# Optimization experiments

Measured on AMD Instinct MI355X. Metric: run time of the kernel, lower is better.

## Reference

```python
import jax, jax.numpy as jnp
import numpy as np

HEAD_SIZE = 64
N_EMBED = 1024
B, T = 8, 2048


def setup_inputs() -> dict:
    key = jax.random.key(0)
    ks = jax.random.split(key, 7)
    s = lambda fan_in: 1.0 / np.sqrt(fan_in)
    return {
        "x": jax.random.normal(ks[0], (B, T, N_EMBED), dtype=jnp.float32),
        # Linear weights stored as (in, out) so projection is x @ W + b
        "Wk": jax.random.uniform(ks[1], (N_EMBED, HEAD_SIZE), jnp.float32, -s(N_EMBED), s(N_EMBED)),
        "bk": jax.random.uniform(ks[2], (HEAD_SIZE,), jnp.float32, -s(N_EMBED), s(N_EMBED)),
        "Wq": jax.random.uniform(ks[3], (N_EMBED, HEAD_SIZE), jnp.float32, -s(N_EMBED), s(N_EMBED)),
        "bq": jax.random.uniform(ks[4], (HEAD_SIZE,), jnp.float32, -s(N_EMBED), s(N_EMBED)),
        "Wv": jax.random.uniform(ks[5], (N_EMBED, HEAD_SIZE), jnp.float32, -s(N_EMBED), s(N_EMBED)),
        "bv": jax.random.uniform(ks[6], (HEAD_SIZE,), jnp.float32, -s(N_EMBED), s(N_EMBED)),
    }


def reference(x, Wk, bk, Wq, bq, Wv, bv):
    Bb, Tt, C = x.shape
    k = x @ Wk + bk  # [B,T,H]
    q = x @ Wq + bq
    v = x @ Wv + bv
    # NOTE: original computes k @ q^T (keys as rows, queries as cols)
    wei = jnp.einsum("bth,bsh->bts", k, q) * (C ** -0.5)  # [B,T,T]
    causal = jnp.tril(jnp.ones((Tt, Tt), dtype=bool))
    wei = jnp.where(causal, wei, -jnp.inf)
    # softplus instead of softmax; softplus(-inf) = 0, stable via logaddexp
    wei = jnp.logaddexp(wei, 0.0)
    # dropout omitted (eval mode / deterministic reference)
    out = jnp.einsum("bts,bsh->bth", wei, v)  # [B,T,H]
    return out
```

## Files before the change

### kernel.cpp

```cpp
#include <hip/hip_runtime.h>
#include <hip/hip_bf16.h>
#include <stdint.h>

#define HEAD 64
#define CEMB 1024
#define BB 8
#define TSEQ 2048

typedef __attribute__((ext_vector_type(8))) short bf16x8;
typedef __attribute__((ext_vector_type(4))) float f32x4;

__device__ __forceinline__ unsigned short f2bf(float f) {
    union { float f; uint32_t u; } c; c.f = f;
    uint32_t u = c.u + 0x7FFF + ((c.u >> 16) & 1);
    return (unsigned short)(u >> 16);
}
__device__ __forceinline__ ushort4 f4bf(float4 v) {
    ushort4 u; u.x = f2bf(v.x); u.y = f2bf(v.y); u.z = f2bf(v.z); u.w = f2bf(v.w);
    return u;
}

__global__ __launch_bounds__(256) void prep_w(
        const float* __restrict__ Wk, const float* __restrict__ bk,
        const float* __restrict__ Wq, const float* __restrict__ bq,
        const float* __restrict__ Wv, const float* __restrict__ bv,
        unsigned short* __restrict__ WTf, float* __restrict__ biasb) {
    __shared__ float Wl[3][32][64];
    const int kc = blockIdx.x;
    const int tid = threadIdx.x;
    const float* Ws[3] = {Wk, Wq, Wv};
    const int row = tid >> 3, cf = (tid & 7) * 8;
    #pragma unroll
    for (int p = 0; p < 3; p++) {
        const float* W = Ws[p] + (long)(kc * 32 + row) * 64 + cf;
        float4 v0 = *(const float4*)(W);
        float4 v1 = *(const float4*)(W + 4);
        *(float4*)(&Wl[p][row][cf]) = v0;
        *(float4*)(&Wl[p][row][cf + 4]) = v1;
    }
    __syncthreads();
    #pragma unroll
    for (int i = 0; i < 3; i++) {
        int cid = i * 256 + tid;
        int lane = cid & 63;
        int l15 = lane & 15, q4 = lane >> 4;
        int n = (cid >> 6) * 16 + l15;
        int p = n >> 6, col = n & 63;
        float scale = (p == 1) ? 0.03125f : 1.0f;
        unsigned short o[8];
        for (int e = 0; e < 8; e++) o[e] = f2bf(Wl[p][q4 * 8 + e][col] * scale);
        *(int4*)(WTf + (long)kc * 6144 + (long)cid * 8) = *(int4*)o;
    }
    if (kc == 0 && tid < 192) {
        const float* bs[3] = {bk, bq, bv};
        int p = tid >> 6;
        biasb[tid] = bs[p][tid & 63] * ((p == 1) ? 0.03125f : 1.0f);
    }
}

__global__ __launch_bounds__(768) void proj_gemm(
        const float* __restrict__ x, const unsigned short* __restrict__ WTf,
        const float* __restrict__ biasb,
        unsigned short* __restrict__ Kb, unsigned short* __restrict__ Qb,
        unsigned short* __restrict__ VTb) {
    __shared__ __align__(16) unsigned short As[64 * 1032];

    const int tid = threadIdx.x;
    const int lane = tid & 63, w = tid >> 6;
    const int l15 = lane & 15, q4 = lane >> 4;
    const long rowbase = (long)blockIdx.x * 64;
    const float* xg = x + rowbase * CEMB;
    const unsigned short* Bg = WTf + w * 512 + (long)lane * 8;

    f32x4 z = {0.f, 0.f, 0.f, 0.f};
    f32x4 acc[4];
    #pragma unroll
    for (int m = 0; m < 4; m++) acc[m] = z;

    bf16x8 Breg[16];

    {
        #pragma unroll
        for (int it = 0; it < 3; it++) {
            int i = it * 768 + tid;
            if (i < 2048) {
                int row = i >> 5, c4 = (i & 31) * 4;
                float4 v = *(const float4*)(xg + row * CEMB + c4);
                *(ushort4*)(As + row * 1032 + c4) = f4bf(v);
            }
        }
    }
    __syncthreads();

    #pragma unroll
    for (int half = 0; half < 2; half++) {
        #pragma unroll
        for (int i = 0; i < 16; i++)
            Breg[i] = *(const bf16x8*)(Bg + (long)(half * 16 + i) * 6144);

        #pragma unroll
        for (int ss = 0; ss < 4; ss++) {
            const int s = half * 4 + ss;
            float4 pf[3];
            if (s < 7) {
                #pragma unroll
                for (int it = 0; it < 3; it++) {
                    int i = it * 768 + tid;
                    if (i < 2048) {
                        int row = i >> 5, c4 = (i & 31) * 4;
                        pf[it] = *(const float4*)(xg + row * CEMB + (s + 1) * 128 + c4);
                    }
                }
            }
            #pragma unroll
            for (int kc = 0; kc < 4; kc++) {
                const int kg = s * 4 + kc;
                #pragma unroll
                for (int m = 0; m < 4; m++) {
                    bf16x8 a = *(const bf16x8*)(As + (m * 16 + l15) * 1032 + kg * 32 + q4 * 8);
                    acc[m] = __builtin_amdgcn_mfma_f32_16x16x32_bf16(a, Breg[ss * 4 + kc], acc[m], 0, 0, 0);
                }
            }
            if (s < 7) {
                #pragma unroll
                for (int it = 0; it < 3; it++) {
                    int i = it * 768 + tid;
                    if (i < 2048) {
                        int row = i >> 5, c4 = (i & 31) * 4;
                        *(ushort4*)(As + row * 1032 + (s + 1) * 128 + c4) = f4bf(pf[it]);
                    }
                }
                __syncthreads();
            }
        }
    }

    const int n = w * 16 + l15;
    const float bias = biasb[n];
    #pragma unroll
    for (int m = 0; m < 4; m++) {
        const long row0 = rowbase + m * 16 + q4 * 4;
        if (n < 128) {
            unsigned short* dst = (n < 64) ? (Kb + row0 * HEAD + n)
                                           : (Qb + row0 * HEAD + (n - 64));
            for (int r = 0; r < 4; r++)
                dst[r * HEAD] = f2bf(acc[m][r] + bias);
        } else {
            const int h = n - 128;
            const long b = row0 >> 11; const int t = (int)(row0 & 2047);
            ushort4 pk;
            pk.x = f2bf(acc[m][0] + bias);
            pk.y = f2bf(acc[m][1] + bias);
            pk.z = f2bf(acc[m][2] + bias);
            pk.w = f2bf(acc[m][3] + bias);
            *(ushort4*)(VTb + b * (HEAD * (long)TSEQ) + (long)h * TSEQ + t) = pk;
        }
    }
}

__global__ __launch_bounds__(512) void attn(
        const unsigned short* __restrict__ Kb, const unsigned short* __restrict__ Qb,
        const unsigned short* __restrict__ VTb, float* __restrict__ out) {
    __shared__ __align__(16) char sm[36864];
    unsigned short* Pl = (unsigned short*)sm;
    float* red = (float*)sm;

    const int tid = threadIdx.x;
    const int lane = tid & 63, w = tid >> 6;
    const int l15 = lane & 15, q4 = lane >> 4;

    const int bid = blockIdx.x;
    const int ti = 63 - (bid >> 3);
    const int b = bid & 7;
    const int t0 = ti * 32;

    const unsigned short* kb  = Kb  + (long)b * TSEQ * HEAD;
    const unsigned short* qb  = Qb  + (long)b * TSEQ * HEAD;
    const unsigned short* vtb = VTb + (long)b * HEAD * TSEQ;

    bf16x8 kf[2][2];
    for (int tt = 0; tt < 2; tt++)
        for (int kk = 0; kk < 2; kk++)
            kf[tt][kk] = *(const bf16x8*)(kb + (t0 + tt * 16 + l15) * HEAD + kk * 32 + q4 * 8);

    f32x4 z = {0.f, 0.f, 0.f, 0.f};
    f32x4 oacc[4][2];
    for (int hh = 0; hh < 4; hh++) for (int tt = 0; tt < 2; tt++) oacc[hh][tt] = z;

    bf16x8 qpf[2][2], vpf[4];
    if (w <= ti) {
        const int s0 = w * 32;
        for (int st2 = 0; st2 < 2; st2++)
            for (int kk = 0; kk < 2; kk++)
                qpf[st2][kk] = *(const bf16x8*)(qb + (s0 + st2 * 16 + l15) * HEAD + kk * 32 + q4 * 8);
        for (int hh = 0; hh < 4; hh++)
            vpf[hh] = *(const bf16x8*)(vtb + (hh * 16 + l15) * (long)TSEQ + s0 + q4 * 8);
    }

    unsigned short* myP = Pl + w * 1280;
    for (int c = w; c <= ti; c += 8) {
        const int s0 = c * 32;

        bf16x8 qf[2][2], vf[4];
        for (int st2 = 0; st2 < 2; st2++)
            for (int kk = 0; kk < 2; kk++) qf[st2][kk] = qpf[st2][kk];
        for (int hh = 0; hh < 4; hh++) vf[hh] = vpf[hh];

        if (c + 8 <= ti) {
            const int sn = (c + 8) * 32;
            for (int st2 = 0; st2 < 2; st2++)
                for (int kk = 0; kk < 2; kk++)
                    qpf[st2][kk] = *(const bf16x8*)(qb + (sn + st2 * 16 + l15) * HEAD + kk * 32 + q4 * 8);
            for (int hh = 0; hh < 4; hh++)
                vpf[hh] = *(const bf16x8*)(vtb + (hh * 16 + l15) * (long)TSEQ + sn + q4 * 8);
        }

        f32x4 sc[2][2];
        for (int st2 = 0; st2 < 2; st2++)
            for (int tt = 0; tt < 2; tt++) {
                f32x4 s = z;
                s = __builtin_amdgcn_mfma_f32_16x16x32_bf16(qf[st2][0], kf[tt][0], s, 0, 0, 0);
                s = __builtin_amdgcn_mfma_f32_16x16x32_bf16(qf[st2][1], kf[tt][1], s, 0, 0, 0);
                sc[st2][tt] = s;
            }
        for (int tt = 0; tt < 2; tt++) {
            const int tg = t0 + tt * 16 + l15;
            for (int st2 = 0; st2 < 2; st2++) {
                ushort4 pk;
                unsigned short pv[4];
                for (int r = 0; r < 4; r++) {
                    int sg = s0 + st2 * 16 + q4 * 4 + r;
                    float p = __logf(1.0f + __expf(sc[st2][tt][r]));
                    if (sg > tg) p = 0.0f;
                    pv[r] = f2bf(p);
                }
                pk.x = pv[0]; pk.y = pv[1]; pk.z = pv[2]; pk.w = pv[3];
                *(ushort4*)(myP + (tt * 16 + l15) * 40 + st2 * 16 + q4 * 4) = pk;
            }
        }
        __threadfence_block();
        bf16x8 pf0 = *(const bf16x8*)(myP + l15 * 40 + q4 * 8);
        bf16x8 pf1 = *(const bf16x8*)(myP + (16 + l15) * 40 + q4 * 8);
        for (int hh = 0; hh < 4; hh++) {
            oacc[hh][0] = __builtin_amdgcn_mfma_f32_16x16x32_bf16(vf[hh], pf0, oacc[hh][0], 0, 0, 0);
            oacc[hh][1] = __builtin_amdgcn_mfma_f32_16x16x32_bf16(vf[hh], pf1, oacc[hh][1], 0, 0, 0);
        }
    }

    __syncthreads();
    if (w >= 4) {
        float* r0 = red + (w - 4) * 2304 + lane * 36;
        for (int hh = 0; hh < 4; hh++)
            for (int tt = 0; tt < 2; tt++)
                *(f32x4*)(r0 + (hh * 2 + tt) * 4) = oacc[hh][tt];
    }
    __syncthreads();
    if (w < 4) {
        const float* r0 = red + w * 2304 + lane * 36;
        for (int hh = 0; hh < 4; hh++)
            for (int tt = 0; tt < 2; tt++)
                oacc[hh][tt] += *(const f32x4*)(r0 + (hh * 2 + tt) * 4);
    }
    __syncthreads();
    if (w == 2 || w == 3) {
        float* r0 = red + (w - 2) * 2304 + lane * 36;
        for (int hh = 0; hh < 4; hh++)
            for (int tt = 0; tt < 2; tt++)
                *(f32x4*)(r0 + (hh * 2 + tt) * 4) = oacc[hh][tt];
    }
    __syncthreads();
    if (w < 2) {
        const float* r0 = red + w * 2304 + lane * 36;
        for (int hh = 0; hh < 4; hh++)
            for (int tt = 0; tt < 2; tt++)
                oacc[hh][tt] += *(const f32x4*)(r0 + (hh * 2 + tt) * 4);
    }
    __syncthreads();
    if (w == 1) {
        float* r0 = red + lane * 36;
        for (int hh = 0; hh < 4; hh++)
            for (int tt = 0; tt < 2; tt++)
                *(f32x4*)(r0 + (hh * 2 + tt) * 4) = oacc[hh][tt];
    }
    __syncthreads();
    if (w == 0) {
        const float* r0 = red + lane * 36;
        for (int hh = 0; hh < 4; hh++)
            for (int tt = 0; tt < 2; tt++)
                oacc[hh][tt] += *(const f32x4*)(r0 + (hh * 2 + tt) * 4);
        for (int tt = 0; tt < 2; tt++) {
            float* ob = out + ((long)b * TSEQ + t0 + tt * 16 + l15) * HEAD + q4 * 4;
            for (int hh = 0; hh < 4; hh++)
                *(f32x4*)(ob + hh * 16) = oacc[hh][tt];
        }
    }
}

extern "C" void kernel_launch(void* const* d_in, const int* in_sizes, int n_in,
                              void* d_out, int out_size, void* d_ws, size_t ws_size,
                              hipStream_t stream) {
    const float* x  = (const float*)d_in[0];
    const float* Wk = (const float*)d_in[1];
    const float* bk = (const float*)d_in[2];
    const float* Wq = (const float*)d_in[3];
    const float* bq = (const float*)d_in[4];
    const float* Wv = (const float*)d_in[5];
    const float* bv = (const float*)d_in[6];
    float* out = (float*)d_out;

    char* ws = (char*)d_ws;
    unsigned short* WTf   = (unsigned short*)(ws);
    float*          biasb = (float*)(ws + 393216);
    unsigned short* Kb    = (unsigned short*)(ws + 524288);
    unsigned short* Qb    = (unsigned short*)(ws + 524288 + 2097152);
    unsigned short* VTb   = (unsigned short*)(ws + 524288 + 4194304);

    prep_w<<<32, 256, 0, stream>>>(Wk, bk, Wq, bq, Wv, bv, WTf, biasb);
    proj_gemm<<<256, 768, 0, stream>>>(x, WTf, biasb, Kb, Qb, VTb);
    attn<<<512, 512, 0, stream>>>(Kb, Qb, VTb, out);
}
```

Baseline: 142.0 us.

## Fuse weight prep, projection GEMM and attention into one cooperative persistent kernel

Merges the three kernel launches into a single cooperative kernel of 256 blocks of 768 threads, with grid-wide syncs between the weight-prep, projection and attention phases. The attention phase now has each block handle two paired query tiles (g and 511-g) to balance the causal workload, uses 12 waves per tile instead of 8, and does a three-level LDS reduction. This removes launch gaps and kernel tails, at the cost of grid-sync overhead, lower occupancy (one block per CU because of the large shared-memory allocation), and 12-wave attention blocks that may schedule less well than the previous 512 blocks.

After: 351.7 us. 148% more time.

```diff
diff --git a/kernel.cpp b/kernel.cpp
--- a/kernel.cpp
+++ b/kernel.cpp
@@ -1,6 +1,9 @@
 #include <hip/hip_runtime.h>
 #include <hip/hip_bf16.h>
+#include <hip/hip_cooperative_groups.h>
 #include <stdint.h>
+
+namespace cg = cooperative_groups;
 
 #define HEAD 64
 #define CEMB 1024
@@ -20,66 +23,76 @@
     return u;
 }
 
-__global__ __launch_bounds__(256) void prep_w(
+__global__ __launch_bounds__(768) void fused_attn(
+        const float* __restrict__ x,
         const float* __restrict__ Wk, const float* __restrict__ bk,
         const float* __restrict__ Wq, const float* __restrict__ bq,
         const float* __restrict__ Wv, const float* __restrict__ bv,
-        unsigned short* __restrict__ WTf, float* __restrict__ biasb) {
-    __shared__ float Wl[3][32][64];
-    const int kc = blockIdx.x;
-    const int tid = threadIdx.x;
-    const float* Ws[3] = {Wk, Wq, Wv};
-    const int row = tid >> 3, cf = (tid & 7) * 8;
-    #pragma unroll
-    for (int p = 0; p < 3; p++) {
-        const float* W = Ws[p] + (long)(kc * 32 + row) * 64 + cf;
-        float4 v0 = *(const float4*)(W);
-        float4 v1 = *(const float4*)(W + 4);
-        *(float4*)(&Wl[p][row][cf]) = v0;
-        *(float4*)(&Wl[p][row][cf + 4]) = v1;
-    }
-    __syncthreads();
-    #pragma unroll
-    for (int i = 0; i < 3; i++) {
-        int cid = i * 256 + tid;
-        int lane = cid & 63;
-        int l15 = lane & 15, q4 = lane >> 4;
-        int n = (cid >> 6) * 16 + l15;
-        int p = n >> 6, col = n & 63;
-        float scale = (p == 1) ? 0.03125f : 1.0f;
-        unsigned short o[8];
-        for (int e = 0; e < 8; e++) o[e] = f2bf(Wl[p][q4 * 8 + e][col] * scale);
-        *(int4*)(WTf + (long)kc * 6144 + (long)cid * 8) = *(int4*)o;
-    }
-    if (kc == 0 && tid < 192) {
-        const float* bs[3] = {bk, bq, bv};
-        int p = tid >> 6;
-        biasb[tid] = bs[p][tid & 63] * ((p == 1) ? 0.03125f : 1.0f);
-    }
-}
-
-__global__ __launch_bounds__(768) void proj_gemm(
-        const float* __restrict__ x, const unsigned short* __restrict__ WTf,
-        const float* __restrict__ biasb,
+        unsigned short* __restrict__ WTf, float* __restrict__ biasb,
         unsigned short* __restrict__ Kb, unsigned short* __restrict__ Qb,
-        unsigned short* __restrict__ VTb) {
-    __shared__ __align__(16) unsigned short As[64 * 1032];
-
+        unsigned short* __restrict__ VTb, float* __restrict__ out) {
+    __shared__ __align__(16) char smem[132096];
+
+    cg::grid_group grid = cg::this_grid();
     const int tid = threadIdx.x;
     const int lane = tid & 63, w = tid >> 6;
     const int l15 = lane & 15, q4 = lane >> 4;
-    const long rowbase = (long)blockIdx.x * 64;
-    const float* xg = x + rowbase * CEMB;
-    const unsigned short* Bg = WTf + w * 512 + (long)lane * 8;
-
-    f32x4 z = {0.f, 0.f, 0.f, 0.f};
-    f32x4 acc[4];
-    #pragma unroll
-    for (int m = 0; m < 4; m++) acc[m] = z;
-
-    bf16x8 Breg[16];
+    const int g = blockIdx.x;
 
     {
+        float* Wl = (float*)smem;
+        if (g < 32 && tid < 256) {
+            const int kc = g;
+            const float* Ws[3] = {Wk, Wq, Wv};
+            const int row = tid >> 3, cf = (tid & 7) * 8;
+            #pragma unroll
+            for (int p = 0; p < 3; p++) {
+                const float* W = Ws[p] + (long)(kc * 32 + row) * 64 + cf;
+                float4 v0 = *(const float4*)(W);
+                float4 v1 = *(const float4*)(W + 4);
+                *(float4*)(Wl + ((p * 32 + row) * 64 + cf)) = v0;
+                *(float4*)(Wl + ((p * 32 + row) * 64 + cf + 4)) = v1;
+            }
+        }
+        __syncthreads();
+        if (g < 32 && tid < 256) {
+            const int kc = g;
+            #pragma unroll
+            for (int i = 0; i < 3; i++) {
+                int cid = i * 256 + tid;
+                int ln = cid & 63;
+                int li = ln & 15, qq = ln >> 4;
+                int n = (cid >> 6) * 16 + li;
+                int p = n >> 6, col = n & 63;
+                float scale = (p == 1) ? 0.03125f : 1.0f;
+                unsigned short o[8];
+                for (int e = 0; e < 8; e++)
+                    o[e] = f2bf(Wl[(p * 32 + qq * 8 + e) * 64 + col] * scale);
+                *(int4*)(WTf + (long)kc * 6144 + (long)cid * 8) = *(int4*)o;
+            }
+            if (kc == 0 && tid < 192) {
+                const float* bs[3] = {bk, bq, bv};
+                int p = tid >> 6;
+                biasb[tid] = bs[p][tid & 63] * ((p == 1) ? 0.03125f : 1.0f);
+            }
+        }
+    }
+    __threadfence();
+    grid.sync();
+
+    {
+        unsigned short* As = (unsigned short*)smem;
+        const long rowbase = (long)g * 64;
+        const float* xg = x + rowbase * CEMB;
+        const unsigned short* Bg = WTf + w * 512 + (long)lane * 8;
+
+        f32x4 z = {0.f, 0.f, 0.f, 0.f};
+        f32x4 acc[4];
+        #pragma unroll
+        for (int m = 0; m < 4; m++) acc[m] = z;
+
+        bf16x8 Breg[16];
+
         #pragma unroll
         for (int it = 0; it < 3; it++) {
             int i = it * 768 + tid;
@@ -89,209 +102,208 @@
                 *(ushort4*)(As + row * 1032 + c4) = f4bf(v);
             }
         }
+        __syncthreads();
+
+        #pragma unroll
+        for (int half = 0; half < 2; half++) {
+            #pragma unroll
+            for (int i = 0; i < 16; i++)
+                Breg[i] = *(const bf16x8*)(Bg + (long)(half * 16 + i) * 6144);
+
+            #pragma unroll
+            for (int ss = 0; ss < 4; ss++) {
+                const int s = half * 4 + ss;
+                float4 pf[3];
+                if (s < 7) {
+                    #pragma unroll
+                    for (int it = 0; it < 3; it++) {
+                        int i = it * 768 + tid;
+                        if (i < 2048) {
+                            int row = i >> 5, c4 = (i & 31) * 4;
+                            pf[it] = *(const float4*)(xg + row * CEMB + (s + 1) * 128 + c4);
+                        }
+                    }
+                }
+                #pragma unroll
+                for (int kc = 0; kc < 4; kc++) {
+                    const int kg = s * 4 + kc;
+                    #pragma unroll
+                    for (int m = 0; m < 4; m++) {
+                        bf16x8 a = *(const bf16x8*)(As + (m * 16 + l15) * 1032 + kg * 32 + q4 * 8);
+                        acc[m] = __builtin_amdgcn_mfma_f32_16x16x32_bf16(a, Breg[ss * 4 + kc], acc[m], 0, 0, 0);
+                    }
+                }
+                if (s < 7) {
+                    #pragma unroll
+                    for (int it = 0; it < 3; it++) {
+                        int i = it * 768 + tid;
+                        if (i < 2048) {
+                            int row = i >> 5, c4 = (i & 31) * 4;
+                            *(ushort4*)(As + row * 1032 + (s + 1) * 128 + c4) = f4bf(pf[it]);
+                        }
+                    }
+                    __syncthreads();
+                }
+            }
+        }
+
+        const int n = w * 16 + l15;
+        const float bias = biasb[n];
+        #pragma unroll
+        for (int m = 0; m < 4; m++) {
+            const long row0 = rowbase + m * 16 + q4 * 4;
+            if (n < 128) {
+                unsigned short* dst = (n < 64) ? (Kb + row0 * HEAD + n)
+                                               : (Qb + row0 * HEAD + (n - 64));
+                for (int r = 0; r < 4; r++)
+                    dst[r * HEAD] = f2bf(acc[m][r] + bias);
+            } else {
+                const int h = n - 128;
+                const long b = row0 >> 11; const int t = (int)(row0 & 2047);
+                ushort4 pk;
+                pk.x = f2bf(acc[m][0] + bias);
+                pk.y = f2bf(acc[m][1] + bias);
+                pk.z = f2bf(acc[m][2] + bias);
+                pk.w = f2bf(acc[m][3] + bias);
+                *(ushort4*)(VTb + b * (HEAD * (long)TSEQ) + (long)h * TSEQ + t) = pk;
+            }
+        }
     }
-    __syncthreads();
-
-    #pragma unroll
-    for (int half = 0; half < 2; half++) {
-        #pragma unroll
-        for (int i = 0; i < 16; i++)
-            Breg[i] = *(const bf16x8*)(Bg + (long)(half * 16 + i) * 6144);
-
-        #pragma unroll
-        for (int ss = 0; ss < 4; ss++) {
-            const int s = half * 4 + ss;
-            float4 pf[3];
-            if (s < 7) {
-                #pragma unroll
-                for (int it = 0; it < 3; it++) {
-                    int i = it * 768 + tid;
-                    if (i < 2048) {
-                        int row = i >> 5, c4 = (i & 31) * 4;
-                        pf[it] = *(const float4*)(xg + row * CEMB + (s + 1) * 128 + c4);
-                    }
-                }
-            }
-            #pragma unroll
-            for (int kc = 0; kc < 4; kc++) {
-                const int kg = s * 4 + kc;
-                #pragma unroll
-                for (int m = 0; m < 4; m++) {
-                    bf16x8 a = *(const bf16x8*)(As + (m * 16 + l15) * 1032 + kg * 32 + q4 * 8);
-                    acc[m] = __builtin_amdgcn_mfma_f32_16x16x32_bf16(a, Breg[ss * 4 + kc], acc[m], 0, 0, 0);
-                }
-            }
-            if (s < 7) {
-                #pragma unroll
-                for (int it = 0; it < 3; it++) {
-                    int i = it * 768 + tid;
-                    if (i < 2048) {
-                        int row = i >> 5, c4 = (i & 31) * 4;
-                        *(ushort4*)(As + row * 1032 + (s + 1) * 128 + c4) = f4bf(pf[it]);
-                    }
-                }
-                __syncthreads();
-            }
-        }
-    }
-
-    const int n = w * 16 + l15;
-    const float bias = biasb[n];
-    #pragma unroll
-    for (int m = 0; m < 4; m++) {
-        const long row0 = rowbase + m * 16 + q4 * 4;
-        if (n < 128) {
-            unsigned short* dst = (n < 64) ? (Kb + row0 * HEAD + n)
-                                           : (Qb + row0 * HEAD + (n - 64));
-            for (int r = 0; r < 4; r++)
-                dst[r * HEAD] = f2bf(acc[m][r] + bias);
-        } else {
-            const int h = n - 128;
-            const long b = row0 >> 11; const int t = (int)(row0 & 2047);
-            ushort4 pk;
-            pk.x = f2bf(acc[m][0] + bias);
-            pk.y = f2bf(acc[m][1] + bias);
-            pk.z = f2bf(acc[m][2] + bias);
-            pk.w = f2bf(acc[m][3] + bias);
-            *(ushort4*)(VTb + b * (HEAD * (long)TSEQ) + (long)h * TSEQ + t) = pk;
-        }
-    }
-}
-
-__global__ __launch_bounds__(512) void attn(
-        const unsigned short* __restrict__ Kb, const unsigned short* __restrict__ Qb,
-        const unsigned short* __restrict__ VTb, float* __restrict__ out) {
-    __shared__ __align__(16) char sm[36864];
-    unsigned short* Pl = (unsigned short*)sm;
-    float* red = (float*)sm;
-
-    const int tid = threadIdx.x;
-    const int lane = tid & 63, w = tid >> 6;
-    const int l15 = lane & 15, q4 = lane >> 4;
-
-    const int bid = blockIdx.x;
-    const int ti = 63 - (bid >> 3);
-    const int b = bid & 7;
-    const int t0 = ti * 32;
-
-    const unsigned short* kb  = Kb  + (long)b * TSEQ * HEAD;
-    const unsigned short* qb  = Qb  + (long)b * TSEQ * HEAD;
-    const unsigned short* vtb = VTb + (long)b * HEAD * TSEQ;
-
-    bf16x8 kf[2][2];
-    for (int tt = 0; tt < 2; tt++)
-        for (int kk = 0; kk < 2; kk++)
-            kf[tt][kk] = *(const bf16x8*)(kb + (t0 + tt * 16 + l15) * HEAD + kk * 32 + q4 * 8);
-
-    f32x4 z = {0.f, 0.f, 0.f, 0.f};
-    f32x4 oacc[4][2];
-    for (int hh = 0; hh < 4; hh++) for (int tt = 0; tt < 2; tt++) oacc[hh][tt] = z;
-
-    bf16x8 qpf[2][2], vpf[4];
-    if (w <= ti) {
-        const int s0 = w * 32;
-        for (int st2 = 0; st2 < 2; st2++)
-            for (int kk = 0; kk < 2; kk++)
-                qpf[st2][kk] = *(const bf16x8*)(qb + (s0 + st2 * 16 + l15) * HEAD + kk * 32 + q4 * 8);
-        for (int hh = 0; hh < 4; hh++)
-            vpf[hh] = *(const bf16x8*)(vtb + (hh * 16 + l15) * (long)TSEQ + s0 + q4 * 8);
-    }
-
-    unsigned short* myP = Pl + w * 1280;
-    for (int c = w; c <= ti; c += 8) {
-        const int s0 = c * 32;
-
-        bf16x8 qf[2][2], vf[4];
-        for (int st2 = 0; st2 < 2; st2++)
-            for (int kk = 0; kk < 2; kk++) qf[st2][kk] = qpf[st2][kk];
-        for (int hh = 0; hh < 4; hh++) vf[hh] = vpf[hh];
-
-        if (c + 8 <= ti) {
-            const int sn = (c + 8) * 32;
-            for (int st2 = 0; st2 < 2; st2++)
+    __threadfence();
+    grid.sync();
+
+    {
+        unsigned short* Pl = (unsigned short*)smem;
+        float* red = (float*)(smem + 30720);
+        unsigned short* myP = Pl + w * 1280;
+
+        #pragma unroll 1
+        for (int jj = 0; jj < 2; jj++) {
+            const int j = jj ? (511 - g) : g;
+            const int ti = 63 - (j >> 3);
+            const int b = j & 7;
+            const int t0 = ti * 32;
+
+            const unsigned short* kb  = Kb  + (long)b * TSEQ * HEAD;
+            const unsigned short* qb  = Qb  + (long)b * TSEQ * HEAD;
+            const unsigned short* vtb = VTb + (long)b * HEAD * TSEQ;
+
+            bf16x8 kf[2][2];
+            for (int tt = 0; tt < 2; tt++)
                 for (int kk = 0; kk < 2; kk++)
-                    qpf[st2][kk] = *(const bf16x8*)(qb + (sn + st2 * 16 + l15) * HEAD + kk * 32 + q4 * 8);
-            for (int hh = 0; hh < 4; hh++)
-                vpf[hh] = *(const bf16x8*)(vtb + (hh * 16 + l15) * (long)TSEQ + sn + q4 * 8);
-        }
-
-        f32x4 sc[2][2];
-        for (int st2 = 0; st2 < 2; st2++)
-            for (int tt = 0; tt < 2; tt++) {
-                f32x4 s = z;
-                s = __builtin_amdgcn_mfma_f32_16x16x32_bf16(qf[st2][0], kf[tt][0], s, 0, 0, 0);
-                s = __builtin_amdgcn_mfma_f32_16x16x32_bf16(qf[st2][1], kf[tt][1], s, 0, 0, 0);
-                sc[st2][tt] = s;
-            }
-        for (int tt = 0; tt < 2; tt++) {
-            const int tg = t0 + tt * 16 + l15;
-            for (int st2 = 0; st2 < 2; st2++) {
-                ushort4 pk;
-                unsigned short pv[4];
-                for (int r = 0; r < 4; r++) {
-                    int sg = s0 + st2 * 16 + q4 * 4 + r;
-                    float p = __logf(1.0f + __expf(sc[st2][tt][r]));
-                    if (sg > tg) p = 0.0f;
-                    pv[r] = f2bf(p);
-                }
-                pk.x = pv[0]; pk.y = pv[1]; pk.z = pv[2]; pk.w = pv[3];
-                *(ushort4*)(myP + (tt * 16 + l15) * 40 + st2 * 16 + q4 * 4) = pk;
-            }
-        }
-        __threadfence_block();
-        bf16x8 pf0 = *(const bf16x8*)(myP + l15 * 40 + q4 * 8);
-        bf16x8 pf1 = *(const bf16x8*)(myP + (16 + l15) * 40 + q4 * 8);
-        for (int hh = 0; hh < 4; hh++) {
-            oacc[hh][0] = __builtin_amdgcn_mfma_f32_16x16x32_bf16(vf[hh], pf0, oacc[hh][0], 0, 0, 0);
-            oacc[hh][1] = __builtin_amdgcn_mfma_f32_16x16x32_bf16(vf[hh], pf1, oacc[hh][1], 0, 0, 0);
-        }
-    }
-
-    __syncthreads();
-    if (w >= 4) {
-        float* r0 = red + (w - 4) * 2304 + lane * 36;
-        for (int hh = 0; hh < 4; hh++)
-            for (int tt = 0; tt < 2; tt++)
-                *(f32x4*)(r0 + (hh * 2 + tt) * 4) = oacc[hh][tt];
-    }
-    __syncthreads();
-    if (w < 4) {
-        const float* r0 = red + w * 2304 + lane * 36;
-        for (int hh = 0; hh < 4; hh++)
-            for (int tt = 0; tt < 2; tt++)
-                oacc[hh][tt] += *(const f32x4*)(r0 + (hh * 2 + tt) * 4);
-    }
-    __syncthreads();
-    if (w == 2 || w == 3) {
-        float* r0 = red + (w - 2) * 2304 + lane * 36;
-        for (int hh = 0; hh < 4; hh++)
-            for (int tt = 0; tt < 2; tt++)
-                *(f32x4*)(r0 + (hh * 2 + tt) * 4) = oacc[hh][tt];
-    }
-    __syncthreads();
-    if (w < 2) {
-        const float* r0 = red + w * 2304 + lane * 36;
-        for (int hh = 0; hh < 4; hh++)
-            for (int tt = 0; tt < 2; tt++)
-                oacc[hh][tt] += *(const f32x4*)(r0 + (hh * 2 + tt) * 4);
-    }
-    __syncthreads();
-    if (w == 1) {
-        float* r0 = red + lane * 36;
-        for (int hh = 0; hh < 4; hh++)
-            for (int tt = 0; tt < 2; tt++)
-                *(f32x4*)(r0 + (hh * 2 + tt) * 4) = oacc[hh][tt];
-    }
-    __syncthreads();
-    if (w == 0) {
-        const float* r0 = red + lane * 36;
-        for (int hh = 0; hh < 4; hh++)
-            for (int tt = 0; tt < 2; tt++)
-                oacc[hh][tt] += *(const f32x4*)(r0 + (hh * 2 + tt) * 4);
-        for (int tt = 0; tt < 2; tt++) {
-            float* ob = out + ((long)b * TSEQ + t0 + tt * 16 + l15) * HEAD + q4 * 4;
-            for (int hh = 0; hh < 4; hh++)
-                *(f32x4*)(ob + hh * 16) = oacc[hh][tt];
+                    kf[tt][kk] = *(const bf16x8*)(kb + (t0 + tt * 16 + l15) * HEAD + kk * 32 + q4 * 8);
+
+            f32x4 z = {0.f, 0.f, 0.f, 0.f};
+            f32x4 oacc[4][2];
+            for (int hh = 0; hh < 4; hh++) for (int tt = 0; tt < 2; tt++) oacc[hh][tt] = z;
+
+            bf16x8 qpf[2][2], vpf[4];
+            if (w <= ti) {
+                const int s0 = w * 32;
+                for (int st2 = 0; st2 < 2; st2++)
+                    for (int kk = 0; kk < 2; kk++)
+                        qpf[st2][kk] = *(const bf16x8*)(qb + (s0 + st2 * 16 + l15) * HEAD + kk * 32 + q4 * 8);
+                for (int hh = 0; hh < 4; hh++)
+                    vpf[hh] = *(const bf16x8*)(vtb + (hh * 16 + l15) * (long)TSEQ + s0 + q4 * 8);
+            }
+
+            for (int c = w; c <= ti; c += 12) {
+                const int s0 = c * 32;
+                bf16x8 qf[2][2], vf[4];
+                for (int st2 = 0; st2 < 2; st2++)
+                    for (int kk = 0; kk < 2; kk++) qf[st2][kk] = qpf[st2][kk];
+                for (int hh = 0; hh < 4; hh++) vf[hh] = vpf[hh];
+
+                if (c + 12 <= ti) {
+                    const int sn = (c + 12) * 32;
+                    for (int st2 = 0; st2 < 2; st2++)
+                        for (int kk = 0; kk < 2; kk++)
+                            qpf[st2][kk] = *(const bf16x8*)(qb + (sn + st2 * 16 + l15) * HEAD + kk * 32 + q4 * 8);
+                    for (int hh = 0; hh < 4; hh++)
+                        vpf[hh] = *(const bf16x8*)(vtb + (hh * 16 + l15) * (long)TSEQ + sn + q4 * 8);
+                }
+
+                f32x4 sc[2][2];
+                for (int st2 = 0; st2 < 2; st2++)
+                    for (int tt = 0; tt < 2; tt++) {
+                        f32x4 s = z;
+                        s = __builtin_amdgcn_mfma_f32_16x16x32_bf16(qf[st2][0], kf[tt][0], s, 0, 0, 0);
+                        s = __builtin_amdgcn_mfma_f32_16x16x32_bf16(qf[st2][1], kf[tt][1], s, 0, 0, 0);
+                        sc[st2][tt] = s;
+                    }
+                for (int tt = 0; tt < 2; tt++) {
+                    const int tg = t0 + tt * 16 + l15;
+                    for (int st2 = 0; st2 < 2; st2++) {
+                        ushort4 pk;
+                        unsigned short pv[4];
+                        for (int r = 0; r < 4; r++) {
+                            int sg = s0 + st2 * 16 + q4 * 4 + r;
+                            float p = __logf(1.0f + __expf(sc[st2][tt][r]));
+                            if (sg > tg) p = 0.0f;
+                            pv[r] = f2bf(p);
+                        }
+                        pk.x = pv[0]; pk.y = pv[1]; pk.z = pv[2]; pk.w = pv[3];
+                        *(ushort4*)(myP + (tt * 16 + l15) * 40 + st2 * 16 + q4 * 4) = pk;
+                    }
+                }
+                __threadfence_block();
+                bf16x8 pf0 = *(const bf16x8*)(myP + l15 * 40 + q4 * 8);
+                bf16x8 pf1 = *(const bf16x8*)(myP + (16 + l15) * 40 + q4 * 8);
+                for (int hh = 0; hh < 4; hh++) {
+                    oacc[hh][0] = __builtin_amdgcn_mfma_f32_16x16x32_bf16(vf[hh], pf0, oacc[hh][0], 0, 0, 0);
+                    oacc[hh][1] = __builtin_amdgcn_mfma_f32_16x16x32_bf16(vf[hh], pf1, oacc[hh][1], 0, 0, 0);
+                }
+            }
+
+            __syncthreads();
+            if (w >= 6) {
+                float* r0 = red + (w - 6) * 2304 + lane * 36;
+                for (int hh = 0; hh < 4; hh++)
+                    for (int tt = 0; tt < 2; tt++)
+                        *(f32x4*)(r0 + (hh * 2 + tt) * 4) = oacc[hh][tt];
+            }
+            __syncthreads();
+            if (w < 6) {
+                const float* r0 = red + w * 2304 + lane * 36;
+                for (int hh = 0; hh < 4; hh++)
+                    for (int tt = 0; tt < 2; tt++)
+                        oacc[hh][tt] += *(const f32x4*)(r0 + (hh * 2 + tt) * 4);
+            }
+            __syncthreads();
+            if (w >= 3 && w < 6) {
+                float* r0 = red + (w - 3) * 2304 + lane * 36;
+                for (int hh = 0; hh < 4; hh++)
+                    for (int tt = 0; tt < 2; tt++)
+                        *(f32x4*)(r0 + (hh * 2 + tt) * 4) = oacc[hh][tt];
+            }
+            __syncthreads();
+            if (w < 3) {
+                const float* r0 = red + w * 2304 + lane * 36;
+                for (int hh = 0; hh < 4; hh++)
+                    for (int tt = 0; tt < 2; tt++)
+                        oacc[hh][tt] += *(const f32x4*)(r0 + (hh * 2 + tt) * 4);
+            }
+            __syncthreads();
+            if (w == 1 || w == 2) {
+                float* r0 = red + (w - 1) * 2304 + lane * 36;
+                for (int hh = 0; hh < 4; hh++)
+                    for (int tt = 0; tt < 2; tt++)
+                        *(f32x4*)(r0 + (hh * 2 + tt) * 4) = oacc[hh][tt];
+            }
+            __syncthreads();
+            if (w == 0) {
+                for (int i = 0; i < 2; i++) {
+                    const float* r0 = red + i * 2304 + lane * 36;
+                    for (int hh = 0; hh < 4; hh++)
+                        for (int tt = 0; tt < 2; tt++)
+                            oacc[hh][tt] += *(const f32x4*)(r0 + (hh * 2 + tt) * 4);
+                }
+                for (int tt = 0; tt < 2; tt++) {
+                    float* ob = out + ((long)b * TSEQ + t0 + tt * 16 + l15) * HEAD + q4 * 4;
+                    for (int hh = 0; hh < 4; hh++)
+                        *(f32x4*)(ob + hh * 16) = oacc[hh][tt];
+                }
+            }
         }
     }
 }
@@ -315,7 +327,9 @@
     unsigned short* Qb    = (unsigned short*)(ws + 524288 + 2097152);
     unsigned short* VTb   = (unsigned short*)(ws + 524288 + 4194304);
 
-    prep_w<<<32, 256, 0, stream>>>(Wk, bk, Wq, bq, Wv, bv, WTf, biasb);
-    proj_gemm<<<256, 768, 0, stream>>>(x, WTf, biasb, Kb, Qb, VTb);
-    attn<<<512, 512, 0, stream>>>(Kb, Qb, VTb, out);
+    void* args[] = {(void*)&x, (void*)&Wk, (void*)&bk, (void*)&Wq, (void*)&bq,
+                    (void*)&Wv, (void*)&bv, (void*)&WTf, (void*)&biasb,
+                    (void*)&Kb, (void*)&Qb, (void*)&VTb, (void*)&out};
+    hipLaunchCooperativeKernel((const void*)fused_attn, dim3(256), dim3(768),
+                               args, 0, stream);
 }
```
